# Kernel tuning notes

Measured on AMD Instinct MI355X. Metric: run time of the kernel, lower is better.

Reference implementation:

```python
import jax, jax.numpy as jnp
import numpy as np

B, NE, NMAX = 256, 90, 270
ZE = PE = GE = PPS = 32
NPROPS = 20
FP, SGE, LATH = 256, 64, 128
PIN = FP + SGE + LATH  # 448 = pred_inp_size = conv input (add_to_node)
C1, C2, H = 448, 256, 3
P1 = P2 = 512
EPS = 1e-5

PNAMES = ['sg_emb_table','lat_W1','lat_b1','lat_bn1_g','lat_bn1_b','lat_bn1_m','lat_bn1_v',
          'lat_W2','lat_b2','lat_bn2_g','lat_bn2_b','lat_bn2_m','lat_bn2_v',
          'z_emb_table','period_table','group_table','props','W_props','b_props','W_phys','b_phys',
          'gat1_W','gat1_as','gat1_ad','gat1_b','gat2_W','gat2_as','gat2_ad','gat2_b',
          'pW1','pb1','pbn1_g','pbn1_b','pbn1_m','pbn1_v',
          'pW2','pb2','pbn2_g','pbn2_b','pbn2_m','pbn2_v','pW3','pb3']

def _bn(x, g, b, m, v):
    return (x - m) * g / jnp.sqrt(v + EPS) + b

def _lrelu(x, s=0.2):
    return jnp.where(x >= 0, x, s * x)

def _gat(x, adj, W, a_s, a_d, bias):
    # PyG DenseGATConv: concat=False (mean over heads), dropout=0, negative_slope=0.2
    Bn, N, _ = x.shape
    h = (x @ W).reshape(Bn, N, H, -1)                      # [B,N,H,C]
    asrc = (h * a_s).sum(-1)                               # [B,N,H]
    adst = (h * a_d).sum(-1)
    alpha = asrc[:, None, :, :] + adst[:, :, None, :]      # [B,i,j,H]
    alpha = _lrelu(alpha, 0.2)
    adj_sl = jnp.maximum(adj, jnp.eye(N, dtype=adj.dtype))  # add self loops
    alpha = jnp.where(adj_sl[..., None] > 0, alpha, -jnp.inf)
    alpha = jax.nn.softmax(alpha, axis=2)                  # softmax over sources j
    out = jnp.einsum('bijh,bjhc->bihc', alpha, h)
    return out.mean(2) + bias                              # [B,N,C]

def _forward(comp, sg, lat, period_idx, group_idx, p):
    sg_x = p['sg_emb_table'][sg[:, 0]]                     # [B,SGE]
    # lattice MLP: (Linear -> BN -> LeakyReLU(True)==identity) x2
    h = _bn(lat @ p['lat_W1'] + p['lat_b1'], p['lat_bn1_g'], p['lat_bn1_b'], p['lat_bn1_m'], p['lat_bn1_v'])
    lat_x = _bn(h @ p['lat_W2'] + p['lat_b2'], p['lat_bn2_g'], p['lat_bn2_b'], p['lat_bn2_m'], p['lat_bn2_v'])
    # ragged -> dense batch: expand composition counts into dense node-type grid
    n_atoms = comp.sum(1)                                  # [B]
    cum = jnp.cumsum(comp, axis=1)                         # [B,NE]
    t = jnp.arange(NMAX)
    z = jax.vmap(lambda c: jnp.searchsorted(c, t, side='right'))(cum)  # [B,NMAX]
    mask = t[None, :] < n_atoms[:, None]                   # [B,NMAX] valid nodes
    z = jnp.where(mask, z, 0)
    # PhysEmbedding: z/period/group embeddings + projected properties -> final proj
    phys = jnp.concatenate([
        p['z_emb_table'][z],
        p['period_table'][period_idx[z]],
        p['group_table'][group_idx[z]],
        p['props'][z] @ p['W_props'] + p['b_props'],
    ], axis=-1)
    phys = phys @ p['W_phys'] + p['b_phys']                # [B,NMAX,FP]
    # add_to_node: cat graph-level lat/sg embeddings onto every node, then zero-pad
    node = jnp.concatenate([
        phys,
        jnp.broadcast_to(lat_x[:, None, :], (lat_x.shape[0], NMAX, LATH)),
        jnp.broadcast_to(sg_x[:, None, :], (sg_x.shape[0], NMAX, SGE)),
    ], axis=-1)
    node = node * mask[..., None].astype(node.dtype)       # to_dense_batch zero padding
    # per-graph dense block adjacency, zero diagonal (fill_diagonal_(0))
    adj = (mask[:, :, None] & mask[:, None, :]).astype(node.dtype)
    adj = adj * (1.0 - jnp.eye(NMAX, dtype=node.dtype))
    # GNNBlock: act = LeakyReLU(True) == identity (negative_slope=1)
    x1 = _gat(node, adj, p['gat1_W'], p['gat1_as'], p['gat1_ad'], p['gat1_b'])
    x2 = _gat(x1, adj, p['gat2_W'], p['gat2_as'], p['gat2_ad'], p['gat2_b'])
    comp_x = x2.sum(1)                                     # sum over ALL NMAX slots (incl. padding, as torch does)
    feat = jnp.concatenate([comp_x, sg_x, lat_x], axis=-1) # [B,PIN]
    # prediction head (eval: dropout off, BN running stats)
    h = _lrelu(_bn(feat @ p['pW1'] + p['pb1'], p['pbn1_g'], p['pbn1_b'], p['pbn1_m'], p['pbn1_v']))
    h = _lrelu(_bn(h @ p['pW2'] + p['pb2'], p['pbn2_g'], p['pbn2_b'], p['pbn2_m'], p['pbn2_v']))
    return h @ p['pW3'] + p['pb3']                         # [B,1]

def setup_inputs():
    key = jax.random.key(0)
    ks = iter(jax.random.split(key, 64))
    def nrm(shape, s=0.05):
        return jax.random.normal(next(ks), shape, dtype=jnp.float32) * s
    comp = jax.random.randint(next(ks), (B, NE), 0, 4, dtype=jnp.int32)
    comp = comp.at[0].set(3)  # graph 0 has exactly NMAX atoms -> data N_max == NMAX
    sg = jax.random.randint(next(ks), (B, 1), 0, 230)
    lat = jax.random.uniform(next(ks), (B, 6), dtype=jnp.float32)
    period_idx = jax.random.randint(next(ks), (NE,), 0, 8)
    group_idx = jax.random.randint(next(ks), (NE,), 0, 19)
    inp = dict(comp=comp, sg=sg, lat=lat, period_idx=period_idx, group_idx=group_idx)
    inp.update(
        sg_emb_table=nrm((230, SGE)),
        lat_W1=nrm((6, LATH)), lat_b1=nrm((LATH,)),
        lat_bn1_g=jnp.ones(LATH), lat_bn1_b=jnp.zeros(LATH), lat_bn1_m=jnp.zeros(LATH), lat_bn1_v=jnp.ones(LATH),
        lat_W2=nrm((LATH, LATH)), lat_b2=nrm((LATH,)),
        lat_bn2_g=jnp.ones(LATH), lat_bn2_b=jnp.zeros(LATH), lat_bn2_m=jnp.zeros(LATH), lat_bn2_v=jnp.ones(LATH),
        z_emb_table=nrm((NE, ZE)), period_table=nrm((8, PE)), group_table=nrm((19, GE)),
        props=nrm((NE, NPROPS), 0.1), W_props=nrm((NPROPS, PPS)), b_props=nrm((PPS,)),
        W_phys=nrm((ZE + PE + GE + PPS, FP)), b_phys=nrm((FP,)),
        gat1_W=nrm((PIN, H * C1)), gat1_as=nrm((H, C1)), gat1_ad=nrm((H, C1)), gat1_b=nrm((C1,)),
        gat2_W=nrm((C1, H * C2)), gat2_as=nrm((H, C2)), gat2_ad=nrm((H, C2)), gat2_b=nrm((C2,)),
        pW1=nrm((PIN, P1)), pb1=nrm((P1,)),
        pbn1_g=jnp.ones(P1), pbn1_b=jnp.zeros(P1), pbn1_m=jnp.zeros(P1), pbn1_v=jnp.ones(P1),
        pW2=nrm((P1, P2)), pb2=nrm((P2,)),
        pbn2_g=jnp.ones(P2), pbn2_b=jnp.zeros(P2), pbn2_m=jnp.zeros(P2), pbn2_v=jnp.ones(P2),
        pW3=nrm((P2, 1)), pb3=nrm((1,)),
    )
    return inp

def reference(comp, sg, lat, period_idx, group_idx,
              sg_emb_table, lat_W1, lat_b1, lat_bn1_g, lat_bn1_b, lat_bn1_m, lat_bn1_v,
              lat_W2, lat_b2, lat_bn2_g, lat_bn2_b, lat_bn2_m, lat_bn2_v,
              z_emb_table, period_table, group_table, props, W_props, b_props, W_phys, b_phys,
              gat1_W, gat1_as, gat1_ad, gat1_b, gat2_W, gat2_as, gat2_ad, gat2_b,
              pW1, pb1, pbn1_g, pbn1_b, pbn1_m, pbn1_v,
              pW2, pb2, pbn2_g, pbn2_b, pbn2_m, pbn2_v, pW3, pb3):
    vals = (sg_emb_table, lat_W1, lat_b1, lat_bn1_g, lat_bn1_b, lat_bn1_m, lat_bn1_v,
            lat_W2, lat_b2, lat_bn2_g, lat_bn2_b, lat_bn2_m, lat_bn2_v,
            z_emb_table, period_table, group_table, props, W_props, b_props, W_phys, b_phys,
            gat1_W, gat1_as, gat1_ad, gat1_b, gat2_W, gat2_as, gat2_ad, gat2_b,
            pW1, pb1, pbn1_g, pbn1_b, pbn1_m, pbn1_v,
            pW2, pb2, pbn2_g, pbn2_b, pbn2_m, pbn2_v, pW3, pb3)
    p = dict(zip(PNAMES, vals))
    return _forward(comp, sg, lat, period_idx, group_idx, p)
```

## Files before the change

### kernel.cpp

```cpp
#include <hip/hip_runtime.h>
#include <math.h>

#define BB 256
#define NEL 90
#define NMAX 270
#define C1 448
#define C2 256
#define PIN 448
#define LATH 128
#define SGE 64
#define P1 512
#define EPSB 1e-5f

typedef short shortx8 __attribute__((ext_vector_type(8)));
typedef float floatx4 __attribute__((ext_vector_type(4)));

__device__ __forceinline__ float bf2f(unsigned short u) {
  return __uint_as_float(((unsigned)u) << 16);
}
__device__ __forceinline__ unsigned short f2bf(float f) {
  unsigned x = __float_as_uint(f);
  unsigned r = (x + 0x7fffu + ((x >> 16) & 1u)) >> 16;
  return (unsigned short)r;
}

__global__ __launch_bounds__(256) void k_prep(
    const int* __restrict__ comp, const int* __restrict__ sg, const float* __restrict__ lat,
    const float* __restrict__ sg_emb,
    const float* __restrict__ W1, const float* __restrict__ b1,
    const float* __restrict__ g1, const float* __restrict__ be1,
    const float* __restrict__ m1, const float* __restrict__ v1,
    const float* __restrict__ W2, const float* __restrict__ b2,
    const float* __restrict__ g2, const float* __restrict__ be2,
    const float* __restrict__ m2, const float* __restrict__ v2,
    float* __restrict__ sgx, float* __restrict__ latx,
    int* __restrict__ z, int* __restrict__ natoms) {
  int b = blockIdx.x;
  int tid = threadIdx.x;
  __shared__ int cum[NEL];
  __shared__ float hbuf[LATH];
  __shared__ float latl[6];
  if (tid == 0) {
    int s = 0;
    for (int e = 0; e < NEL; ++e) { s += comp[b * NEL + e]; cum[e] = s; }
    natoms[b] = s;
  }
  if (tid < 6) latl[tid] = lat[b * 6 + tid];
  __syncthreads();
  int n = cum[NEL - 1];
  for (int t = tid; t < NMAX; t += blockDim.x) {
    int zz = -1;
    if (t < n) {
      for (int e = 0; e < NEL; ++e) { if (cum[e] > t) { zz = e; break; } }
    }
    z[b * NMAX + t] = zz;
  }
  if (tid < SGE) {
    int si = sg[b];
    sgx[b * SGE + tid] = sg_emb[si * SGE + tid];
  }
  if (tid < LATH) {
    float acc = b1[tid];
    for (int k = 0; k < 6; ++k) acc += latl[k] * W1[k * LATH + tid];
    acc = (acc - m1[tid]) * g1[tid] * rsqrtf(v1[tid] + EPSB) + be1[tid];
    hbuf[tid] = acc;
  }
  __syncthreads();
  if (tid < LATH) {
    float acc = b2[tid];
    for (int k = 0; k < LATH; ++k) acc += hbuf[k] * W2[k * LATH + tid];
    acc = (acc - m2[tid]) * g2[tid] * rsqrtf(v2[tid] + EPSB) + be2[tid];
    latx[b * LATH + tid] = acc;
  }
}

__global__ __launch_bounds__(256) void k_scan(const int* __restrict__ natoms,
                                              int* __restrict__ off,
                                              int* __restrict__ aoff) {
  __shared__ int sh[BB];
  int tid = threadIdx.x;
  int v0 = natoms[tid];
  sh[tid] = v0;
  for (int d = 1; d < BB; d <<= 1) {
    __syncthreads();
    int v = (tid >= d) ? sh[tid - d] : 0;
    __syncthreads();
    sh[tid] += v;
  }
  __syncthreads();
  off[tid] = sh[tid] - v0;
  __syncthreads();
  int sz = 3 * ((((v0 + 15) >> 4) << 4)) * ((((v0 + 31) >> 5) << 5));
  sh[tid] = sz;
  for (int d = 1; d < BB; d <<= 1) {
    __syncthreads();
    int v = (tid >= d) ? sh[tid - d] : 0;
    __syncthreads();
    sh[tid] += v;
  }
  __syncthreads();
  aoff[tid] = sh[tid] - sz;
}

__global__ __launch_bounds__(256) void k_physpe(
    const int* __restrict__ period_idx, const int* __restrict__ group_idx,
    const float* __restrict__ z_emb, const float* __restrict__ period_t,
    const float* __restrict__ group_t, const float* __restrict__ props,
    const float* __restrict__ Wp, const float* __restrict__ bp,
    const float* __restrict__ Wphys, const float* __restrict__ bphys,
    float* __restrict__ physpe) {
  int e = blockIdx.x;
  int tid = threadIdx.x;
  __shared__ float ph[128];
  if (tid < 32) ph[tid] = z_emb[e * 32 + tid];
  else if (tid < 64) ph[tid] = period_t[period_idx[e] * 32 + tid - 32];
  else if (tid < 96) ph[tid] = group_t[group_idx[e] * 32 + tid - 64];
  else if (tid < 128) {
    int j = tid - 96;
    float acc = bp[j];
    for (int k = 0; k < 20; ++k) acc += props[e * 20 + k] * Wp[k * 32 + j];
    ph[tid] = acc;
  }
  __syncthreads();
  float acc = bphys[tid];
  for (int k = 0; k < 128; ++k) acc += ph[k] * Wphys[k * 256 + tid];
  physpe[e * 256 + tid] = acc;
}

__global__ __launch_bounds__(256) void k_nodep(
    const int* __restrict__ z, const int* __restrict__ off, const int* __restrict__ natoms,
    const float* __restrict__ physpe, const float* __restrict__ latx,
    const float* __restrict__ sgx, unsigned short* __restrict__ x0) {
  int b = blockIdx.x;
  int n = natoms[b], ob = off[b];
  int tid = threadIdx.x;
  __shared__ int zl[NMAX];
  for (int t = tid; t < n; t += 256) zl[t] = z[b * NMAX + t];
  __syncthreads();
  int items = n * 56;
  for (int e = tid; e < items; e += 256) {
    int t = e / 56, c8 = (e - t * 56) << 3;
    int zt = zl[t];
    float v[8];
    if (c8 < 256) {
      float4 a = *(const float4*)(physpe + zt * 256 + c8);
      float4 c = *(const float4*)(physpe + zt * 256 + c8 + 4);
      v[0] = a.x; v[1] = a.y; v[2] = a.z; v[3] = a.w;
      v[4] = c.x; v[5] = c.y; v[6] = c.z; v[7] = c.w;
    } else if (c8 < 384) {
      float4 a = *(const float4*)(latx + b * LATH + c8 - 256);
      float4 c = *(const float4*)(latx + b * LATH + c8 - 252);
      v[0] = a.x; v[1] = a.y; v[2] = a.z; v[3] = a.w;
      v[4] = c.x; v[5] = c.y; v[6] = c.z; v[7] = c.w;
    } else {
      float4 a = *(const float4*)(sgx + b * SGE + c8 - 384);
      float4 c = *(const float4*)(sgx + b * SGE + c8 - 380);
      v[0] = a.x; v[1] = a.y; v[2] = a.z; v[3] = a.w;
      v[4] = c.x; v[5] = c.y; v[6] = c.z; v[7] = c.w;
    }
    unsigned short u[8];
    #pragma unroll
    for (int i = 0; i < 8; ++i) u[i] = f2bf(v[i]);
    *(uint4*)(x0 + (size_t)(ob + t) * PIN + c8) = *(uint4*)u;
  }
}

__global__ __launch_bounds__(256) void k_wprep(
    const float* __restrict__ W, unsigned short* __restrict__ Wt, int K, int NC3) {
  int k0 = blockIdx.x << 5;
  int c0 = blockIdx.y << 5;
  __shared__ float ts[32][33];
  int e = threadIdx.x << 2;
  int kk = e >> 5, cc = e & 31;
  float4 v = *(const float4*)(W + (size_t)(k0 + kk) * NC3 + c0 + cc);
  ts[kk][cc] = v.x; ts[kk][cc + 1] = v.y; ts[kk][cc + 2] = v.z; ts[kk][cc + 3] = v.w;
  __syncthreads();
  int c2 = threadIdx.x & 31, kg = threadIdx.x >> 5;
  ushort4 u;
  u.x = f2bf(ts[kg * 4 + 0][c2]); u.y = f2bf(ts[kg * 4 + 1][c2]);
  u.z = f2bf(ts[kg * 4 + 2][c2]); u.w = f2bf(ts[kg * 4 + 3][c2]);
  *(ushort4*)(Wt + (size_t)(c0 + c2) * K + k0 + (kg << 2)) = u;
}

__global__ __launch_bounds__(64) void k_fold(
    const float* __restrict__ W, const float* __restrict__ a_s, const float* __restrict__ a_d,
    int NC3, int C, float* __restrict__ wsv, float* __restrict__ wdv) {
  int k = blockIdx.x;
  int tid = threadIdx.x;
  for (int h = 0; h < 3; ++h) {
    float ss = 0.f, sd = 0.f;
    for (int c = tid; c < C; c += 64) {
      float wv = W[(size_t)k * NC3 + h * C + c];
      ss += wv * a_s[h * C + c];
      sd += wv * a_d[h * C + c];
    }
    for (int o = 32; o > 0; o >>= 1) { ss += __shfl_down(ss, o); sd += __shfl_down(sd, o); }
    if (tid == 0) { wsv[k * 3 + h] = ss; wdv[k * 3 + h] = sd; }
  }
}

__global__ __launch_bounds__(256) void k_av2(
    const unsigned short* __restrict__ x, const float* __restrict__ wsv,
    const float* __restrict__ wdv, const int* __restrict__ off,
    const int* __restrict__ natoms, float* __restrict__ asrc,
    float* __restrict__ adst, int K) {
  __shared__ float sw[C1 * 3], dw[C1 * 3];
  int tid = threadIdx.x;
  for (int e = tid; e < K * 3; e += 256) { sw[e] = wsv[e]; dw[e] = wdv[e]; }
  __syncthreads();
  int total = off[BB - 1] + natoms[BB - 1];
  int row = blockIdx.x * 256 + tid;
  if (row >= total) return;
  const unsigned short* xr = x + (size_t)row * K;
  float s0 = 0.f, s1 = 0.f, s2 = 0.f, d0 = 0.f, d1 = 0.f, d2 = 0.f;
  for (int k = 0; k < K; k += 8) {
    uint4 raw = *(const uint4*)(xr + k);
    unsigned short us[8];
    *(uint4*)us = raw;
    #pragma unroll
    for (int u = 0; u < 8; ++u) {
      float xv = bf2f(us[u]);
      int kb = (k + u) * 3;
      s0 += xv * sw[kb + 0]; s1 += xv * sw[kb + 1]; s2 += xv * sw[kb + 2];
      d0 += xv * dw[kb + 0]; d1 += xv * dw[kb + 1]; d2 += xv * dw[kb + 2];
    }
  }
  asrc[row * 3 + 0] = s0; asrc[row * 3 + 1] = s1; asrc[row * 3 + 2] = s2;
  adst[row * 3 + 0] = d0; adst[row * 3 + 1] = d1; adst[row * 3 + 2] = d2;
}

#define MTMAX 17
__global__ __launch_bounds__(256) void k_alpha(
    const float* __restrict__ asrc, const float* __restrict__ adst,
    const int* __restrict__ off, const int* __restrict__ natoms,
    const int* __restrict__ aoff, unsigned short* __restrict__ alpha) {
  int bid = blockIdx.x;
  int b = bid & (BB - 1);
  int hm = bid >> 8;
  int h = hm % 3;
  int mt = hm / 3;
  int n = natoms[b];
  if (n == 0) return;
  int mtn = (n + 15) >> 4;
  if (mt >= mtn) return;
  int ktn = (n + 31) >> 5;
  int rext = mtn << 4, kext = ktn << 5;
  int ob = off[b];
  size_t ab = (size_t)aoff[b] + (size_t)h * rext * kext;
  int tid = threadIdx.x;
  int wv = tid >> 6, lane = tid & 63;
  __shared__ float asl[288];
  for (int j = tid; j < kext; j += 256)
    asl[j] = (j < n) ? asrc[(ob + j) * 3 + h] : 0.f;
  __syncthreads();
  #pragma unroll
  for (int r = 0; r < 4; ++r) {
    int i = (mt << 4) + (wv << 2) + r;
    unsigned short* rowp = alpha + ab + (size_t)i * kext;
    if (i >= n) {
      for (int j = lane; j < kext; j += 64) rowp[j] = 0;
      continue;
    }
    float ad = adst[(ob + i) * 3 + h];
    float m = -1e30f;
    for (int j = lane; j < n; j += 64) {
      float sc = asl[j] + ad;
      sc = fmaxf(sc, 0.2f * sc);
      m = fmaxf(m, sc);
    }
    for (int o = 32; o > 0; o >>= 1) m = fmaxf(m, __shfl_xor(m, o));
    float s = 0.f;
    for (int j = lane; j < n; j += 64) {
      float sc = asl[j] + ad;
      sc = fmaxf(sc, 0.2f * sc);
      s += __expf(sc - m);
    }
    for (int o = 32; o > 0; o >>= 1) s += __shfl_xor(s, o);
    float rs = 1.f / s;
    for (int j = lane; j < kext; j += 64) {
      float v = 0.f;
      if (j < n) {
        float sc = asl[j] + ad;
        sc = fmaxf(sc, 0.2f * sc);
        v = __expf(sc - m) * rs;
      }
      rowp[j] = f2bf(v);
    }
  }
}

#define MTW 5

__global__ __launch_bounds__(256, 2) void k_fused_mfma(
    const unsigned short* __restrict__ xin, const unsigned short* __restrict__ Wt,
    const unsigned short* __restrict__ alpha, const int* __restrict__ aoff,
    const int* __restrict__ off, const int* __restrict__ natoms,
    const float* __restrict__ bias, unsigned short* __restrict__ xout,
    int K, int C, int NC) {
  int bid = blockIdx.x;
  int xg = bid & 7;
  int g = bid >> 3;
  int cblk = g % NC;
  int b = xg + ((g / NC) << 3);
  int c0 = cblk << 6;
  int n = natoms[b];
  if (n == 0) return;
  int ob = off[b];
  size_t ab = (size_t)aoff[b];
  int tid = threadIdx.x;
  int wv = tid >> 6;
  int lane = tid & 63;
  int m16 = lane & 15;
  int q = lane >> 4;

  int mtn = (n + 15) >> 4;
  int jmax = mtn << 4;
  int ktn = (n + 31) >> 5;
  int kext = ktn << 5;
  size_t hstride = (size_t)jmax * kext;

  __shared__ unsigned short xs[17 * 512];
  __shared__ unsigned short tt[36 * 512];
  unsigned short* wt_s = tt;

  floatx4 acc[MTW][4];
  #pragma unroll
  for (int i = 0; i < MTW; ++i)
    #pragma unroll
    for (int nt = 0; nt < 4; ++nt) acc[i][nt] = (floatx4)0.f;

  for (int h = 0; h < 3; ++h) {
    floatx4 tac[MTW][4];
    #pragma unroll
    for (int i = 0; i < MTW; ++i)
      #pragma unroll
      for (int nt = 0; nt < 4; ++nt) tac[i][nt] = (floatx4)0.f;

    for (int k0 = 0; k0 < K; k0 += 32) {
      __syncthreads();
      for (int e = tid << 3; e < (jmax << 5); e += 2048) {
        int j = e >> 5, kk = e & 31;
        uint4 v = make_uint4(0u, 0u, 0u, 0u);
        if (j < n) v = *(const uint4*)(xin + (size_t)(ob + j) * K + k0 + kk);
        *(uint4*)(xs + ((((j >> 4) << 2) + (kk >> 3)) << 7) + ((j & 15) << 3)) = v;
      }
      {
        int r = tid >> 2, kk = (tid & 3) << 3;
        uint4 wv4 = *(const uint4*)(Wt + (size_t)(h * C + c0 + r) * K + k0 + kk);
        *(uint4*)(wt_s + ((kk >> 3) << 9) + (r << 3)) = wv4;
      }
      __syncthreads();
      shortx8 bfr[4];
      #pragma unroll
      for (int nt = 0; nt < 4; ++nt)
        bfr[nt] = *(const shortx8*)(wt_s + (q << 9) + (((nt << 4) + m16) << 3));
      #pragma unroll
      for (int t_i = 0; t_i < MTW; ++t_i) {
        int mt = wv + (t_i << 2);
        if (mt < mtn) {
          shortx8 a = *(const shortx8*)(xs + ((((mt << 2) + q) << 7)) + (m16 << 3));
          #pragma unroll
          for (int nt = 0; nt < 4; ++nt)
            tac[t_i][nt] = __builtin_amdgcn_mfma_f32_16x16x32_bf16(a, bfr[nt], tac[t_i][nt], 0, 0, 0);
        }
      }
    }
    __syncthreads();
    #pragma unroll
    for (int t_i = 0; t_i < MTW; ++t_i) {
      int mt = wv + (t_i << 2);
      if (mt < mtn) {
        int jbase = (mt << 4) + (q << 2);
        #pragma unroll
        for (int nt = 0; nt < 4; ++nt) {
          floatx4 d = tac[t_i][nt];
          ushort4 u;
          u.x = f2bf(d.x); u.y = f2bf(d.y); u.z = f2bf(d.z); u.w = f2bf(d.w);
          int c = (nt << 4) + m16;
          *(ushort4*)(tt + ((jbase >> 3) << 9) + (c << 3) + (jbase & 7)) = u;
        }
      }
    }
    for (int e = tid; e < ((kext - jmax) << 6); e += 256) {
      int j = jmax + (e >> 6), c = e & 63;
      tt[((j >> 3) << 9) + (c << 3) + (j & 7)] = 0;
    }
    __syncthreads();
    const unsigned short* ap = alpha + ab + (size_t)h * hstride;
    for (int k0p = 0; k0p < kext; k0p += 32) {
      shortx8 tb[4];
      #pragma unroll
      for (int nt = 0; nt < 4; ++nt)
        tb[nt] = *(const shortx8*)(tt + (((k0p >> 3) + q) << 9) + (((nt << 4) + m16) << 3));
      #pragma unroll
      for (int t_i = 0; t_i < MTW; ++t_i) {
        int mt = wv + (t_i << 2);
        if (mt < mtn) {
          shortx8 af = *(const shortx8*)(ap + (size_t)((mt << 4) + m16) * kext + k0p + (q << 3));
          #pragma unroll
          for (int nt = 0; nt < 4; ++nt)
            acc[t_i][nt] = __builtin_amdgcn_mfma_f32_16x16x32_bf16(af, tb[nt], acc[t_i][nt], 0, 0, 0);
        }
      }
    }
    __syncthreads();
  }
  float bq[4];
  #pragma unroll
  for (int nt = 0; nt < 4; ++nt) bq[nt] = bias[c0 + (nt << 4) + m16];
  const float inv3 = 1.f / 3.f;
  #pragma unroll
  for (int t_i = 0; t_i < MTW; ++t_i) {
    int mt = wv + (t_i << 2);
    if (mt < mtn) {
      #pragma unroll
      for (int nt = 0; nt < 4; ++nt) {
        floatx4 d = acc[t_i][nt];
        int cidx = c0 + (nt << 4) + m16;
        #pragma unroll
        for (int r = 0; r < 4; ++r) {
          int i = (mt << 4) + (q << 2) + r;
          if (i < n) xout[(size_t)(ob + i) * C + cidx] = f2bf(d[r] * inv3 + bq[nt]);
        }
      }
    }
  }
}

__global__ __launch_bounds__(128) void k_pad(
    const float* __restrict__ b1, const float* __restrict__ W2,
    const float* __restrict__ b2g, float* __restrict__ pad2) {
  int c = blockIdx.x;
  int tid = threadIdx.x;
  float s = 0.f;
  for (int k = tid; k < C1; k += 128) {
    float bv = b1[k];
    const float* wr = W2 + (size_t)k * (3 * C2) + c;
    s += bv * (wr[0] + wr[C2] + wr[2 * C2]);
  }
  __shared__ float red[128];
  red[tid] = s;
  __syncthreads();
  for (int st = 64; st > 0; st >>= 1) {
    if (tid < st) red[tid] += red[tid + st];
    __syncthreads();
  }
  if (tid == 0) pad2[c] = red[0] * (1.f / 3.f) + b2g[c];
}

__global__ __launch_bounds__(256) void k_feat2(
    const unsigned short* __restrict__ x2, const float* __restrict__ pad2,
    const int* __restrict__ off, const int* __restrict__ natoms,
    const float* __restrict__ sgx, const float* __restrict__ latx,
    float* __restrict__ feat) {
  int b = blockIdx.x, tid = threadIdx.x;
  int n = natoms[b], ob = off[b];
  float s = (float)(NMAX - n) * pad2[tid];
  for (int i = 0; i < n; ++i) s += bf2f(x2[(size_t)(ob + i) * C2 + tid]);
  feat[b * PIN + tid] = s;
  if (tid < SGE) feat[b * PIN + 256 + tid] = sgx[b * SGE + tid];
  if (tid < LATH) feat[b * PIN + 320 + tid] = latx[b * LATH + tid];
}

__global__ __launch_bounds__(256) void k_head(
    const float* __restrict__ feat,
    const float* __restrict__ W1, const float* __restrict__ b1,
    const float* __restrict__ g1, const float* __restrict__ be1,
    const float* __restrict__ m1, const float* __restrict__ v1,
    const float* __restrict__ W2, const float* __restrict__ b2,
    const float* __restrict__ g2, const float* __restrict__ be2,
    const float* __restrict__ m2, const float* __restrict__ v2,
    const float* __restrict__ W3, const float* __restrict__ b3,
    float* __restrict__ out) {
  int b = blockIdx.x, tid = threadIdx.x;
  __shared__ float f[PIN];
  __shared__ float h1[P1];
  __shared__ float h2[P1];
  __shared__ float red[256];
  for (int i = tid; i < PIN; i += 256) f[i] = feat[b * PIN + i];
  __syncthreads();
  for (int o = tid; o < P1; o += 256) {
    float acc = b1[o];
    for (int k = 0; k < PIN; ++k) acc += f[k] * W1[k * P1 + o];
    acc = (acc - m1[o]) * g1[o] * rsqrtf(v1[o] + EPSB) + be1[o];
    h1[o] = acc >= 0.f ? acc : 0.2f * acc;
  }
  __syncthreads();
  for (int o = tid; o < P1; o += 256) {
    float acc = b2[o];
    for (int k = 0; k < P1; ++k) acc += h1[k] * W2[k * P1 + o];
    acc = (acc - m2[o]) * g2[o] * rsqrtf(v2[o] + EPSB) + be2[o];
    h2[o] = acc >= 0.f ? acc : 0.2f * acc;
  }
  __syncthreads();
  float p = 0.f;
  for (int k = tid; k < P1; k += 256) p += h2[k] * W3[k];
  red[tid] = p;
  __syncthreads();
  for (int s = 128; s > 0; s >>= 1) {
    if (tid < s) red[tid] += red[tid + s];
    __syncthreads();
  }
  if (tid == 0) out[b] = red[0] + b3[0];
}

extern "C" void kernel_launch(void* const* d_in, const int* in_sizes, int n_in,
                              void* d_out, int out_size, void* d_ws, size_t ws_size,
                              hipStream_t stream) {
  const int*   comp       = (const int*)d_in[0];
  const int*   sg         = (const int*)d_in[1];
  const float* lat        = (const float*)d_in[2];
  const int*   period_idx = (const int*)d_in[3];
  const int*   group_idx  = (const int*)d_in[4];
  const float* sg_emb     = (const float*)d_in[5];
  const float* lat_W1     = (const float*)d_in[6];
  const float* lat_b1     = (const float*)d_in[7];
  const float* lat_bn1_g  = (const float*)d_in[8];
  const float* lat_bn1_b  = (const float*)d_in[9];
  const float* lat_bn1_m  = (const float*)d_in[10];
  const float* lat_bn1_v  = (const float*)d_in[11];
  const float* lat_W2     = (const float*)d_in[12];
  const float* lat_b2     = (const float*)d_in[13];
  const float* lat_bn2_g  = (const float*)d_in[14];
  const float* lat_bn2_b  = (const float*)d_in[15];
  const float* lat_bn2_m  = (const float*)d_in[16];
  const float* lat_bn2_v  = (const float*)d_in[17];
  const float* z_emb      = (const float*)d_in[18];
  const float* period_t   = (const float*)d_in[19];
  const float* group_t    = (const float*)d_in[20];
  const float* props      = (const float*)d_in[21];
  const float* W_props    = (const float*)d_in[22];
  const float* b_props    = (const float*)d_in[23];
  const float* W_phys     = (const float*)d_in[24];
  const float* b_phys     = (const float*)d_in[25];
  const float* gat1_W     = (const float*)d_in[26];
  const float* gat1_as    = (const float*)d_in[27];
  const float* gat1_ad    = (const float*)d_in[28];
  const float* gat1_b     = (const float*)d_in[29];
  const float* gat2_W     = (const float*)d_in[30];
  const float* gat2_as    = (const float*)d_in[31];
  const float* gat2_ad    = (const float*)d_in[32];
  const float* gat2_b     = (const float*)d_in[33];
  const float* pW1        = (const float*)d_in[34];
  const float* pb1        = (const float*)d_in[35];
  const float* pbn1_g     = (const float*)d_in[36];
  const float* pbn1_b     = (const float*)d_in[37];
  const float* pbn1_m     = (const float*)d_in[38];
  const float* pbn1_v     = (const float*)d_in[39];
  const float* pW2        = (const float*)d_in[40];
  const float* pb2        = (const float*)d_in[41];
  const float* pbn2_g     = (const float*)d_in[42];
  const float* pbn2_b     = (const float*)d_in[43];
  const float* pbn2_m     = (const float*)d_in[44];
  const float* pbn2_v     = (const float*)d_in[45];
  const float* pW3        = (const float*)d_in[46];
  const float* pb3        = (const float*)d_in[47];

  float* ws = (float*)d_ws;
  const size_t o_sgx  = 0;
  const size_t o_latx = o_sgx  + (size_t)BB * SGE;
  const size_t o_nat  = o_latx + (size_t)BB * LATH;
  const size_t o_off  = o_nat  + BB;
  const size_t o_aoff = o_off  + BB;
  const size_t o_z    = o_aoff + BB;
  const size_t o_phys = o_z    + (size_t)BB * NMAX;
  const size_t o_wsv  = o_phys + (size_t)NEL * 256;
  const size_t o_wdv  = o_wsv  + (size_t)C1 * 3;
  const size_t o_asrc = o_wdv  + (size_t)C1 * 3;
  const size_t o_adst = o_asrc + (size_t)BB * NMAX * 3;
  const size_t o_pad2 = o_adst + (size_t)BB * NMAX * 3;
  const size_t o_wt1  = o_pad2 + 256;
  const size_t o_wt2  = o_wt1  + (size_t)(3 * C1) * PIN / 2;
  const size_t o_x0   = o_wt2  + (size_t)(3 * C2) * C1 / 2;
  const size_t o_x1   = o_x0   + (size_t)BB * NMAX * PIN / 2;
  const size_t o_alph = o_x1   + (size_t)BB * NMAX * PIN / 2;

  float* sgx    = ws + o_sgx;
  float* latx   = ws + o_latx;
  int*   natoms = (int*)(ws + o_nat);
  int*   off    = (int*)(ws + o_off);
  int*   aoff   = (int*)(ws + o_aoff);
  int*   z      = (int*)(ws + o_z);
  float* physpe = ws + o_phys;
  float* wsv    = ws + o_wsv;
  float* wdv    = ws + o_wdv;
  float* asrc   = ws + o_asrc;
  float* adst   = ws + o_adst;
  float* pad2   = ws + o_pad2;
  unsigned short* wt1   = (unsigned short*)(ws + o_wt1);
  unsigned short* wt2   = (unsigned short*)(ws + o_wt2);
  unsigned short* x0    = (unsigned short*)(ws + o_x0);
  unsigned short* x1    = (unsigned short*)(ws + o_x1);
  unsigned short* x2    = x0;
  unsigned short* alpha = (unsigned short*)(ws + o_alph);
  float* feat   = ws + o_x1;

  const int AVG = (BB * NMAX + 255) / 256;
  const int ALG = BB * 3 * MTMAX;

  k_prep<<<BB, 256, 0, stream>>>(comp, sg, lat, sg_emb,
      lat_W1, lat_b1, lat_bn1_g, lat_bn1_b, lat_bn1_m, lat_bn1_v,
      lat_W2, lat_b2, lat_bn2_g, lat_bn2_b, lat_bn2_m, lat_bn2_v,
      sgx, latx, z, natoms);
  k_scan<<<1, 256, 0, stream>>>(natoms, off, aoff);
  k_physpe<<<NEL, 256, 0, stream>>>(period_idx, group_idx, z_emb, period_t, group_t,
      props, W_props, b_props, W_phys, b_phys, physpe);
  k_nodep<<<BB, 256, 0, stream>>>(z, off, natoms, physpe, latx, sgx, x0);

  k_wprep<<<dim3(PIN / 32, (3 * C1) / 32), 256, 0, stream>>>(gat1_W, wt1, PIN, 3 * C1);
  k_wprep<<<dim3(C1 / 32, (3 * C2) / 32), 256, 0, stream>>>(gat2_W, wt2, C1, 3 * C2);
  k_pad<<<256, 128, 0, stream>>>(gat1_b, gat2_W, gat2_b, pad2);

  k_fold<<<C1, 64, 0, stream>>>(gat1_W, gat1_as, gat1_ad, 3 * C1, C1, wsv, wdv);
  k_av2<<<AVG, 256, 0, stream>>>(x0, wsv, wdv, off, natoms, asrc, adst, PIN);
  k_alpha<<<ALG, 256, 0, stream>>>(asrc, adst, off, natoms, aoff, alpha);
  k_fused_mfma<<<(C1 / 64) * BB, 256, 0, stream>>>(x0, wt1, alpha, aoff,
      off, natoms, gat1_b, x1, PIN, C1, C1 / 64);

  k_fold<<<C1, 64, 0, stream>>>(gat2_W, gat2_as, gat2_ad, 3 * C2, C2, wsv, wdv);
  k_av2<<<AVG, 256, 0, stream>>>(x1, wsv, wdv, off, natoms, asrc, adst, C1);
  k_alpha<<<ALG, 256, 0, stream>>>(asrc, adst, off, natoms, aoff, alpha);
  k_fused_mfma<<<(C2 / 64) * BB, 256, 0, stream>>>(x1, wt2, alpha, aoff,
      off, natoms, gat2_b, x2, C1, C2, C2 / 64);

  k_feat2<<<BB, 256, 0, stream>>>(x2, pad2, off, natoms, sgx, latx, feat);
  k_head<<<BB, 256, 0, stream>>>(feat,
      pW1, pb1, pbn1_g, pbn1_b, pbn1_m, pbn1_v,
      pW2, pb2, pbn2_g, pbn2_b, pbn2_m, pbn2_v,
      pW3, pb3, (float*)d_out);
}
```

Before: 890.7 us.

## Prefetch GAT operand tiles into registers and parallelize readout and head kernels

```diff
diff --git a/kernel.cpp b/kernel.cpp
--- a/kernel.cpp
+++ b/kernel.cpp
@@ -290,6 +290,7 @@
 }
 
 #define MTW 5
+#define PXN 5
 
 __global__ __launch_bounds__(256, 2) void k_fused_mfma(
     const unsigned short* __restrict__ xin, const unsigned short* __restrict__ Wt,
@@ -318,6 +319,7 @@
   int ktn = (n + 31) >> 5;
   int kext = ktn << 5;
   size_t hstride = (size_t)jmax * kext;
+  const int xlim = jmax << 5;
 
   __shared__ unsigned short xs[17 * 512];
   __shared__ unsigned short tt[36 * 512];
@@ -328,6 +330,8 @@
   for (int i = 0; i < MTW; ++i)
     #pragma unroll
     for (int nt = 0; nt < 4; ++nt) acc[i][nt] = (floatx4)0.f;
+
+  int wr = tid >> 2, wkk = (tid & 3) << 3;
 
   for (int h = 0; h < 3; ++h) {
     floatx4 tac[MTW][4];
@@ -336,20 +340,46 @@
       #pragma unroll
       for (int nt = 0; nt < 4; ++nt) tac[i][nt] = (floatx4)0.f;
 
+    uint4 px[PXN];
+    uint4 pw;
+    #pragma unroll
+    for (int it = 0; it < PXN; ++it) {
+      int e = (tid << 3) + (it << 11);
+      if (e < xlim) {
+        int j = e >> 5, kk = e & 31;
+        uint4 v = make_uint4(0u, 0u, 0u, 0u);
+        if (j < n) v = *(const uint4*)(xin + (size_t)(ob + j) * K + kk);
+        px[it] = v;
+      }
+    }
+    pw = *(const uint4*)(Wt + (size_t)(h * C + c0 + wr) * K + wkk);
+
     for (int k0 = 0; k0 < K; k0 += 32) {
       __syncthreads();
-      for (int e = tid << 3; e < (jmax << 5); e += 2048) {
-        int j = e >> 5, kk = e & 31;
-        uint4 v = make_uint4(0u, 0u, 0u, 0u);
-        if (j < n) v = *(const uint4*)(xin + (size_t)(ob + j) * K + k0 + kk);
-        *(uint4*)(xs + ((((j >> 4) << 2) + (kk >> 3)) << 7) + ((j & 15) << 3)) = v;
-      }
-      {
-        int r = tid >> 2, kk = (tid & 3) << 3;
-        uint4 wv4 = *(const uint4*)(Wt + (size_t)(h * C + c0 + r) * K + k0 + kk);
-        *(uint4*)(wt_s + ((kk >> 3) << 9) + (r << 3)) = wv4;
-      }
+      #pragma unroll
+      for (int it = 0; it < PXN; ++it) {
+        int e = (tid << 3) + (it << 11);
+        if (e < xlim) {
+          int j = e >> 5, kk = e & 31;
+          *(uint4*)(xs + ((((j >> 4) << 2) + (kk >> 3)) << 7) + ((j & 15) << 3)) = px[it];
+        }
+      }
+      *(uint4*)(wt_s + ((wkk >> 3) << 9) + (wr << 3)) = pw;
       __syncthreads();
+      int k1 = k0 + 32;
+      if (k1 < K) {
+        #pragma unroll
+        for (int it = 0; it < PXN; ++it) {
+          int e = (tid << 3) + (it << 11);
+          if (e < xlim) {
+            int j = e >> 5, kk = e & 31;
+            uint4 v = make_uint4(0u, 0u, 0u, 0u);
+            if (j < n) v = *(const uint4*)(xin + (size_t)(ob + j) * K + k1 + kk);
+            px[it] = v;
+          }
+        }
+        pw = *(const uint4*)(Wt + (size_t)(h * C + c0 + wr) * K + k1 + wkk);
+      }
       shortx8 bfr[4];
       #pragma unroll
       for (int nt = 0; nt < 4; ++nt)
@@ -387,20 +417,39 @@
     }
     __syncthreads();
     const unsigned short* ap = alpha + ab + (size_t)h * hstride;
+    shortx8 afc[MTW], afn[MTW];
+    #pragma unroll
+    for (int t_i = 0; t_i < MTW; ++t_i) {
+      int mt = wv + (t_i << 2);
+      if (mt < mtn)
+        afc[t_i] = *(const shortx8*)(ap + (size_t)((mt << 4) + m16) * kext + (q << 3));
+    }
     for (int k0p = 0; k0p < kext; k0p += 32) {
       shortx8 tb[4];
       #pragma unroll
       for (int nt = 0; nt < 4; ++nt)
         tb[nt] = *(const shortx8*)(tt + (((k0p >> 3) + q) << 9) + (((nt << 4) + m16) << 3));
+      int k1p = k0p + 32;
+      if (k1p < kext) {
+        #pragma unroll
+        for (int t_i = 0; t_i < MTW; ++t_i) {
+          int mt = wv + (t_i << 2);
+          if (mt < mtn)
+            afn[t_i] = *(const shortx8*)(ap + (size_t)((mt << 4) + m16) * kext + k1p + (q << 3));
+        }
+      }
       #pragma unroll
       for (int t_i = 0; t_i < MTW; ++t_i) {
         int mt = wv + (t_i << 2);
         if (mt < mtn) {
-          shortx8 af = *(const shortx8*)(ap + (size_t)((mt << 4) + m16) * kext + k0p + (q << 3));
           #pragma unroll
           for (int nt = 0; nt < 4; ++nt)
-            acc[t_i][nt] = __builtin_amdgcn_mfma_f32_16x16x32_bf16(af, tb[nt], acc[t_i][nt], 0, 0, 0);
+            acc[t_i][nt] = __builtin_amdgcn_mfma_f32_16x16x32_bf16(afc[t_i], tb[nt], acc[t_i][nt], 0, 0, 0);
         }
+      }
+      if (k1p < kext) {
+        #pragma unroll
+        for (int t_i = 0; t_i < MTW; ++t_i) afc[t_i] = afn[t_i];
       }
     }
     __syncthreads();
@@ -453,16 +502,25 @@
     const int* __restrict__ off, const int* __restrict__ natoms,
     const float* __restrict__ sgx, const float* __restrict__ latx,
     float* __restrict__ feat) {
-  int b = blockIdx.x, tid = threadIdx.x;
+  int b = blockIdx.y;
+  int chunk = blockIdx.x;
+  int tid = threadIdx.x;
   int n = natoms[b], ob = off[b];
-  float s = (float)(NMAX - n) * pad2[tid];
-  for (int i = 0; i < n; ++i) s += bf2f(x2[(size_t)(ob + i) * C2 + tid]);
-  feat[b * PIN + tid] = s;
-  if (tid < SGE) feat[b * PIN + 256 + tid] = sgx[b * SGE + tid];
-  if (tid < LATH) feat[b * PIN + 320 + tid] = latx[b * LATH + tid];
-}
-
-__global__ __launch_bounds__(256) void k_head(
+  if (chunk == 17) {
+    atomicAdd(&feat[b * PIN + tid], (float)(NMAX - n) * pad2[tid]);
+    if (tid < SGE) feat[b * PIN + 256 + tid] = sgx[b * SGE + tid];
+    if (tid < LATH) feat[b * PIN + 320 + tid] = latx[b * LATH + tid];
+    return;
+  }
+  int i0 = chunk << 4;
+  if (i0 >= n) return;
+  int i1 = min(i0 + 16, n);
+  float s = 0.f;
+  for (int i = i0; i < i1; ++i) s += bf2f(x2[(size_t)(ob + i) * C2 + tid]);
+  atomicAdd(&feat[b * PIN + tid], s);
+}
+
+__global__ __launch_bounds__(512) void k_head(
     const float* __restrict__ feat,
     const float* __restrict__ W1, const float* __restrict__ b1,
     const float* __restrict__ g1, const float* __restrict__ be1,
@@ -476,28 +534,28 @@
   __shared__ float f[PIN];
   __shared__ float h1[P1];
   __shared__ float h2[P1];
-  __shared__ float red[256];
-  for (int i = tid; i < PIN; i += 256) f[i] = feat[b * PIN + i];
-  __syncthreads();
-  for (int o = tid; o < P1; o += 256) {
+  __shared__ float red[512];
+  for (int i = tid; i < PIN; i += 512) f[i] = feat[b * PIN + i];
+  __syncthreads();
+  {
+    int o = tid;
     float acc = b1[o];
     for (int k = 0; k < PIN; ++k) acc += f[k] * W1[k * P1 + o];
     acc = (acc - m1[o]) * g1[o] * rsqrtf(v1[o] + EPSB) + be1[o];
     h1[o] = acc >= 0.f ? acc : 0.2f * acc;
   }
   __syncthreads();
-  for (int o = tid; o < P1; o += 256) {
+  {
+    int o = tid;
     float acc = b2[o];
     for (int k = 0; k < P1; ++k) acc += h1[k] * W2[k * P1 + o];
     acc = (acc - m2[o]) * g2[o] * rsqrtf(v2[o] + EPSB) + be2[o];
     h2[o] = acc >= 0.f ? acc : 0.2f * acc;
   }
   __syncthreads();
-  float p = 0.f;
-  for (int k = tid; k < P1; k += 256) p += h2[k] * W3[k];
-  red[tid] = p;
-  __syncthreads();
-  for (int s = 128; s > 0; s >>= 1) {
+  red[tid] = h2[tid] * W3[tid];
+  __syncthreads();
+  for (int s = 256; s > 0; s >>= 1) {
     if (tid < s) red[tid] += red[tid + s];
     __syncthreads();
   }
@@ -623,8 +681,9 @@
   k_fused_mfma<<<(C2 / 64) * BB, 256, 0, stream>>>(x1, wt2, alpha, aoff,
       off, natoms, gat2_b, x2, C1, C2, C2 / 64);
 
-  k_feat2<<<BB, 256, 0, stream>>>(x2, pad2, off, natoms, sgx, latx, feat);
-  k_head<<<BB, 256, 0, stream>>>(feat,
+  hipMemsetAsync(feat, 0, (size_t)BB * PIN * sizeof(float), stream);
+  k_feat2<<<dim3(18, BB), 256, 0, stream>>>(x2, pad2, off, natoms, sgx, latx, feat);
+  k_head<<<BB, 512, 0, stream>>>(feat,
       pW1, pb1, pbn1_g, pbn1_b, pbn1_m, pbn1_v,
       pW2, pb2, pbn2_g, pbn2_b, pbn2_m, pbn2_v,
       pW3, pb3, (float*)d_out);
```

New measurement: 944.6 us. +6.1%, slower.
